# Performance work log

Measured on AMD Instinct MI355X. Metric: run time of the kernel, lower is better.

## Reference

```python
import jax, jax.numpy as jnp
import numpy as np

N_NODES = 100000
N_EDGES = 1600000
N_GRAPHS = 2000
F_IN = 16
HEADS = 8
C = 16            # per-head out channels (hidden_dim)
HC = HEADS * C    # 128
N_CLASSES = 2
NEG_SLOPE = 0.2   # PyG GATConv default leaky_relu slope


def setup_inputs() -> dict:
    key = jax.random.key(0)
    ks = jax.random.split(key, 12)
    x = jax.random.normal(ks[0], (N_NODES, F_IN), dtype=jnp.float32)
    edge_index = jax.random.randint(ks[1], (2, N_EDGES), 0, N_NODES, dtype=jnp.int32)
    batch = jnp.sort(jax.random.randint(ks[2], (N_NODES,), 0, N_GRAPHS, dtype=jnp.int32))
    s1 = 1.0 / np.sqrt(F_IN)
    s2 = 1.0 / np.sqrt(HC)
    return {
        "x": x,
        "edge_index": edge_index,
        "batch": batch,
        "W1": jax.random.normal(ks[3], (F_IN, HC), dtype=jnp.float32) * s1,
        "a1_src": jax.random.normal(ks[4], (HEADS, C), dtype=jnp.float32) * s2,
        "a1_dst": jax.random.normal(ks[5], (HEADS, C), dtype=jnp.float32) * s2,
        "b1": jnp.zeros((HC,), dtype=jnp.float32),
        "W2": jax.random.normal(ks[6], (HC, HC), dtype=jnp.float32) * s2,
        "a2_src": jax.random.normal(ks[7], (HEADS, C), dtype=jnp.float32) * s2,
        "a2_dst": jax.random.normal(ks[8], (HEADS, C), dtype=jnp.float32) * s2,
        "b2": jnp.zeros((HC,), dtype=jnp.float32),
        "lin_W": jax.random.normal(ks[9], (HC, N_CLASSES), dtype=jnp.float32) * s2,
        "lin_b": jnp.zeros((N_CLASSES,), dtype=jnp.float32),
    }


def gat_layer(h_in, src, dst, W, a_src, a_dst, b, num_nodes):
    # h: [N, H, C] per-head transformed features
    h = (h_in @ W).reshape(num_nodes, HEADS, C)
    # per-node attention half-logits: [N, H]
    logit_src = jnp.einsum('nhc,hc->nh', h, a_src)
    logit_dst = jnp.einsum('nhc,hc->nh', h, a_dst)
    # per-edge logits [E, H]
    e = jax.nn.leaky_relu(logit_src[src] + logit_dst[dst], NEG_SLOPE)
    # segment softmax over incoming edges of each destination node
    m = jax.ops.segment_max(e, dst, num_segments=num_nodes)
    m = jnp.where(jnp.isfinite(m), m, 0.0)
    ex = jnp.exp(e - m[dst])
    denom = jax.ops.segment_sum(ex, dst, num_segments=num_nodes)
    alpha = ex / jnp.maximum(denom[dst], 1e-16)
    # weighted scatter-add aggregation: [N, H, C]
    out = jax.ops.segment_sum(alpha[:, :, None] * h[src], dst, num_segments=num_nodes)
    return out.reshape(num_nodes, HC) + b


def reference(x, edge_index, batch, W1, a1_src, a1_dst, b1, W2, a2_src, a2_dst, b2, lin_W, lin_b):
    n = x.shape[0]
    # PyG GATConv adds self-loops by default
    loops = jnp.arange(n, dtype=edge_index.dtype)
    src = jnp.concatenate([edge_index[0], loops])
    dst = jnp.concatenate([edge_index[1], loops])
    h = jax.nn.relu(gat_layer(x, src, dst, W1, a1_src, a1_dst, b1, n))
    h = jax.nn.relu(gat_layer(h, src, dst, W2, a2_src, a2_dst, b2, n))
    # global mean pool per graph
    sums = jax.ops.segment_sum(h, batch, num_segments=N_GRAPHS)
    counts = jax.ops.segment_sum(jnp.ones((n, 1), h.dtype), batch, num_segments=N_GRAPHS)
    pooled = sums / jnp.maximum(counts, 1.0)
    logits = pooled @ lin_W + lin_b
    return jax.nn.softmax(logits, axis=1)
```

## Files before the change

kernel.cpp:

```cpp
#include <hip/hip_runtime.h>
#include <math.h>

#define N_NODES 100000
#define N_EDGESI 1600000
#define E_TOTAL (N_EDGESI + N_NODES)
#define N_GRAPHS 2000
#define F_IN 16
#define HEADS 8
#define CPH 16
#define HC 128
#define NEG 0.2f

#define BSHIFT 9
#define BNODES (1<<BSHIFT)
#define NBUK ((N_NODES + BNODES - 1)/BNODES)
#define BCAP 12288
#define BIN_EPT 8
#define BIN_TPB 256
#define BIN_EPB (BIN_EPT*BIN_TPB)
#define NBIN_BLK ((E_TOTAL + BIN_EPB - 1)/BIN_EPB)

#define GOFF_BLK ((N_NODES+255)/256)
#define WCONV_BLK ((HC*HC)/256)
#define XCONV_BLK ((N_NODES*4 + 255)/256)
#define W1CONV_BLK ((HC*32)/256)

typedef __bf16 bf16x8 __attribute__((ext_vector_type(8)));
typedef float  f32x4  __attribute__((ext_vector_type(4)));

__device__ __forceinline__ float leaky(float x){ return fmaxf(x, NEG*x); }
__device__ __forceinline__ float bf2f(unsigned short u){ return __uint_as_float(((unsigned)u)<<16); }
__device__ __forceinline__ unsigned short f2bf(float f){
  unsigned u = __float_as_uint(f);
  unsigned r = (u + 0x7fffu + ((u>>16)&1u)) >> 16;
  return (unsigned short)r;
}
__device__ __forceinline__ float blo(unsigned u){ return __uint_as_float(u<<16); }
__device__ __forceinline__ float bhi(unsigned u){ return __uint_as_float(u & 0xffff0000u); }

__global__ void k_pre(const int* __restrict__ ei, int* __restrict__ gpos, unsigned* __restrict__ gbin,
                      const int* __restrict__ batch, int* __restrict__ goff,
                      const float* __restrict__ W2, unsigned short* __restrict__ w2t,
                      const float* __restrict__ x, unsigned short* __restrict__ xbf,
                      const float* __restrict__ W1, unsigned short* __restrict__ w1t){
  int blk = blockIdx.x;
  if (blk < NBIN_BLK){
    __shared__ int cnt[NBUK];
    __shared__ int lofs[NBUK];
    __shared__ int bbase[NBUK];
    __shared__ int ws[4];
    __shared__ unsigned sorted[BIN_EPB];
    __shared__ unsigned short sbkt[BIN_EPB];
    int t = threadIdx.x;
    for (int i = t; i < NBUK; i += BIN_TPB) cnt[i] = 0;
    __syncthreads();
    int base = blk*BIN_EPB;
    unsigned entry[BIN_EPT]; int ebkt[BIN_EPT]; int erank[BIN_EPT];
    #pragma unroll
    for (int i = 0; i < BIN_EPT; ++i){
      int e = base + i*BIN_TPB + t;
      if (e < E_TOTAL){
        unsigned s, d;
        if (e < N_EDGESI){ s = (unsigned)ei[e]; d = (unsigned)ei[N_EDGESI + e]; }
        else { s = d = (unsigned)(e - N_EDGESI); }
        int b = (int)(d >> BSHIFT);
        erank[i] = atomicAdd(&cnt[b], 1);
        ebkt[i] = b;
        entry[i] = ((d & (BNODES-1u)) << 17) | s;
      } else ebkt[i] = -1;
    }
    __syncthreads();
    {
      int lane = t & 63, wv = t >> 6;
      int v = (t < NBUK) ? cnt[t] : 0;
      int sc = v;
      #pragma unroll
      for (int o = 1; o < 64; o <<= 1){ int u = __shfl_up(sc, o, 64); if (lane >= o) sc += u; }
      if (lane == 63) ws[wv] = sc;
      __syncthreads();
      if (wv == 0 && lane < 4){
        int w2v = ws[lane];
        #pragma unroll
        for (int o = 1; o < 4; o <<= 1){ int u = __shfl_up(w2v, o, 64); if (lane >= o) w2v += u; }
        ws[lane] = w2v;
      }
      __syncthreads();
      if (t < NBUK){
        lofs[t] = (wv ? ws[wv-1] : 0) + sc - v;
        bbase[t] = v ? atomicAdd(&gpos[t], v) : 0;
      }
    }
    __syncthreads();
    #pragma unroll
    for (int i = 0; i < BIN_EPT; ++i){
      if (ebkt[i] >= 0){
        int p = lofs[ebkt[i]] + erank[i];
        sorted[p] = entry[i];
        sbkt[p] = (unsigned short)ebkt[i];
      }
    }
    __syncthreads();
    int nval = E_TOTAL - base; if (nval > BIN_EPB) nval = BIN_EPB;
    for (int i = t; i < nval; i += BIN_TPB){
      int b = sbkt[i];
      gbin[(size_t)b*BCAP + bbase[b] + (i - lofs[b])] = sorted[i];
    }
  } else if (blk < NBIN_BLK + GOFF_BLK){
    int n = (blk - NBIN_BLK)*256 + threadIdx.x;
    if (n >= N_NODES) return;
    int b = batch[n];
    if (n == 0){ for (int g = 0; g <= b; ++g) goff[g] = 0; }
    int b1 = (n+1 < N_NODES) ? batch[n+1] : N_GRAPHS;
    for (int g = b+1; g <= b1; ++g) goff[g] = n+1;
  } else if (blk < NBIN_BLK + GOFF_BLK + WCONV_BLK){
    int i = (blk - NBIN_BLK - GOFF_BLK)*256 + threadIdx.x;
    if (i >= HC*HC) return;
    int c = i >> 7, k = i & 127;
    w2t[i] = f2bf(W2[k*HC + c]);
  } else if (blk < NBIN_BLK + GOFF_BLK + WCONV_BLK + XCONV_BLK){
    int p = (blk - NBIN_BLK - GOFF_BLK - WCONV_BLK)*256 + threadIdx.x;
    if (p >= N_NODES*4) return;
    int n = p >> 2, q = p & 3;
    float4 xv = ((const float4*)(x + n*F_IN))[q];
    ushort4 o; o.x = f2bf(xv.x); o.y = f2bf(xv.y); o.z = f2bf(xv.z); o.w = f2bf(xv.w);
    ((ushort4*)(xbf + (size_t)n*32))[q] = o;
    ushort4 z; z.x = 0; z.y = 0; z.z = 0; z.w = 0;
    ((ushort4*)(xbf + (size_t)n*32 + 16))[q] = z;
  } else {
    int i = (blk - NBIN_BLK - GOFF_BLK - WCONV_BLK - XCONV_BLK)*256 + threadIdx.x;
    if (i >= HC*32) return;
    int c = i >> 5, k = i & 31;
    w1t[i] = (k < F_IN) ? f2bf(W1[k*HC + c]) : (unsigned short)0;
  }
}

__global__ __launch_bounds__(512) void k_csr(
                      const int* __restrict__ gpos, const unsigned* __restrict__ gbin,
                      int* __restrict__ off, int* __restrict__ csrc){
  __shared__ int lcnt[BNODES];
  __shared__ int wsum[8];
  __shared__ int gp[NBUK];
  __shared__ int sbase;
  int b = blockIdx.x, t = threadIdx.x;
  for (int i = t; i < NBUK; i += 512) gp[i] = gpos[i];
  lcnt[t] = 0;
  __syncthreads();
  if (t == 0){ int s = 0; for (int j = 0; j < b; ++j) s += gp[j]; sbase = s; }
  int nb = gp[b];
  const unsigned* bb = gbin + (size_t)b*BCAP;
  __syncthreads();
  int base = sbase;
  for (int i = t; i < nb; i += 512) atomicAdd(&lcnt[bb[i] >> 17], 1);
  __syncthreads();
  int lane = t & 63, wv = t >> 6;
  int v = lcnt[t];
  int sc = v;
  #pragma unroll
  for (int o = 1; o < 64; o <<= 1){ int u = __shfl_up(sc, o, 64); if (lane >= o) sc += u; }
  if (lane == 63) wsum[wv] = sc;
  __syncthreads();
  if (wv == 0 && lane < 8){
    int w2 = wsum[lane];
    #pragma unroll
    for (int o = 1; o < 8; o <<= 1){ int u = __shfl_up(w2, o, 64); if (lane >= o) w2 += u; }
    wsum[lane] = w2;
  }
  __syncthreads();
  int excl = (wv ? wsum[wv-1] : 0) + sc - v;
  int d = (b << BSHIFT) + t;
  if (d < N_NODES) off[d] = base + excl;
  if (b == NBUK-1 && t == 0) off[N_NODES] = E_TOTAL;
  __syncthreads();
  lcnt[t] = base + excl;
  __syncthreads();
  for (int i = t; i < nb; i += 512){
    unsigned en = bb[i];
    int p = atomicAdd(&lcnt[en >> 17], 1);
    csrc[p] = (int)(en & 0x1ffffu);
  }
}

template<int KS>
__global__ __launch_bounds__(256) void k_gemm_mfma(
                             const unsigned short* __restrict__ hin,
                             const unsigned short* __restrict__ wt,
                             const float* __restrict__ asrc, const float* __restrict__ adst,
                             unsigned short* __restrict__ hb,
                             float* __restrict__ ls, float* __restrict__ ld){
  __shared__ unsigned short hls[64][132];
  const int KST = KS*32;
  int t = threadIdx.x, lane = t & 63, wv = t >> 6;
  int n0 = blockIdx.x*64 + wv*16;
  int rowl = lane & 15, kgrp = lane >> 4;
  int row = n0 + rowl;
  int rowc = (row < N_NODES) ? row : (N_NODES-1);
  bf16x8 a[KS];
  #pragma unroll
  for (int ks = 0; ks < KS; ++ks)
    a[ks] = *(const bf16x8*)(hin + (size_t)rowc*KST + ks*32 + kgrp*8);
  #pragma unroll
  for (int ct = 0; ct < 8; ++ct){
    f32x4 acc = {0.f, 0.f, 0.f, 0.f};
    int col = ct*16 + rowl;
    #pragma unroll
    for (int ks = 0; ks < KS; ++ks){
      bf16x8 b = *(const bf16x8*)(wt + (size_t)col*KST + ks*32 + kgrp*8);
      acc = __builtin_amdgcn_mfma_f32_16x16x32_bf16(a[ks], b, acc, 0, 0, 0);
    }
    #pragma unroll
    for (int r = 0; r < 4; ++r){
      int lrow = wv*16 + kgrp*4 + r;
      int ro = n0 + kgrp*4 + r;
      unsigned short hv = f2bf(acc[r]);
      hls[lrow][col] = hv;
      if (ro < N_NODES) hb[(size_t)ro*HC + col] = hv;
    }
  }
  __syncthreads();
  #pragma unroll
  for (int pp = 0; pp < 2; ++pp){
    int p = t + pp*256;
    int lrow = p >> 3, h = p & 7;
    int gn = blockIdx.x*64 + lrow;
    if (gn < N_NODES){
      const unsigned short* rp = &hls[lrow][h*16];
      uint2 A = *(const uint2*)rp;
      uint2 B = *(const uint2*)(rp+4);
      uint2 C = *(const uint2*)(rp+8);
      uint2 D = *(const uint2*)(rp+12);
      float c[16] = { blo(A.x), bhi(A.x), blo(A.y), bhi(A.y),
                      blo(B.x), bhi(B.x), blo(B.y), bhi(B.y),
                      blo(C.x), bhi(C.x), blo(C.y), bhi(C.y),
                      blo(D.x), bhi(D.x), blo(D.y), bhi(D.y) };
      const float* as = asrc + h*CPH;
      const float* ad = adst + h*CPH;
      float s0 = 0.f, s1 = 0.f;
      #pragma unroll
      for (int q = 0; q < 16; ++q){ s0 += c[q]*as[q]; s1 += c[q]*ad[q]; }
      ls[gn*8 + h] = s0;
      ld[gn*8 + h] = s1;
    }
  }
}

__global__ void k_agg(const int* __restrict__ off, const int* __restrict__ csrc,
                      const unsigned short* __restrict__ hb, const float* __restrict__ ls,
                      const float* __restrict__ ld, const float* __restrict__ bias,
                      unsigned short* __restrict__ outb){
  int wid = threadIdx.x >> 6, lane = threadIdx.x & 63;
  int n = blockIdx.x*4 + wid;
  if (n >= N_NODES) return;
  int rs = __builtin_amdgcn_readfirstlane(off[n]);
  int re = __builtin_amdgcn_readfirstlane(off[n+1]);
  int q = lane >> 4;
  int l = lane & 15;
  int h = l >> 1;
  float ldh = ld[n*8 + h];
  const uint4* hb4 = (const uint4*)hb;
  float ac0=0.f, ac1=0.f, ac2=0.f, ac3=0.f, ac4=0.f, ac5=0.f, ac6=0.f, ac7=0.f, dsum=0.f;
  #define AGG_BODY(J) { \
    int s = __shfl(sv, (J), 64); \
    float g = ls[s*8 + h]; \
    float ex = __expf(leaky(g + ldh)); \
    uint4 v = hb4[(size_t)s*16 + l]; \
    ac0 += ex*blo(v.x); ac1 += ex*bhi(v.x); \
    ac2 += ex*blo(v.y); ac3 += ex*bhi(v.y); \
    ac4 += ex*blo(v.z); ac5 += ex*bhi(v.z); \
    ac6 += ex*blo(v.w); ac7 += ex*bhi(v.w); \
    dsum += ex; }
  int nb = re - rs;
  for (int cb = 0; cb < nb; cb += 64){
    int cnt = nb - cb; if (cnt > 64) cnt = 64;
    int sv = csrc[rs + cb + (lane < cnt ? lane : 0)];
    int jj = 0;
    for (; jj + 16 <= cnt; jj += 16){
      AGG_BODY(jj+q) AGG_BODY(jj+q+4) AGG_BODY(jj+q+8) AGG_BODY(jj+q+12)
    }
    for (int j = jj + q; j < cnt; j += 4) AGG_BODY(j)
  }
  #undef AGG_BODY
  ac0 += __shfl_xor(ac0,16,64); ac0 += __shfl_xor(ac0,32,64);
  ac1 += __shfl_xor(ac1,16,64); ac1 += __shfl_xor(ac1,32,64);
  ac2 += __shfl_xor(ac2,16,64); ac2 += __shfl_xor(ac2,32,64);
  ac3 += __shfl_xor(ac3,16,64); ac3 += __shfl_xor(ac3,32,64);
  ac4 += __shfl_xor(ac4,16,64); ac4 += __shfl_xor(ac4,32,64);
  ac5 += __shfl_xor(ac5,16,64); ac5 += __shfl_xor(ac5,32,64);
  ac6 += __shfl_xor(ac6,16,64); ac6 += __shfl_xor(ac6,32,64);
  ac7 += __shfl_xor(ac7,16,64); ac7 += __shfl_xor(ac7,32,64);
  dsum += __shfl_xor(dsum,16,64); dsum += __shfl_xor(dsum,32,64);
  if (q == 0){
    float inv = 1.f/fmaxf(dsum, 1e-16f);
    float4 b0 = ((const float4*)bias)[l*2];
    float4 b1 = ((const float4*)bias)[l*2+1];
    uint4 o;
    o.x = (unsigned)f2bf(fmaxf(ac0*inv + b0.x, 0.f)) | ((unsigned)f2bf(fmaxf(ac1*inv + b0.y, 0.f)) << 16);
    o.y = (unsigned)f2bf(fmaxf(ac2*inv + b0.z, 0.f)) | ((unsigned)f2bf(fmaxf(ac3*inv + b0.w, 0.f)) << 16);
    o.z = (unsigned)f2bf(fmaxf(ac4*inv + b1.x, 0.f)) | ((unsigned)f2bf(fmaxf(ac5*inv + b1.y, 0.f)) << 16);
    o.w = (unsigned)f2bf(fmaxf(ac6*inv + b1.z, 0.f)) | ((unsigned)f2bf(fmaxf(ac7*inv + b1.w, 0.f)) << 16);
    ((uint4*)outb)[(size_t)n*16 + l] = o;
  }
}

__global__ void k_poolcls(const unsigned short* __restrict__ h, const int* __restrict__ goff,
                          const float* __restrict__ lw, const float* __restrict__ lb,
                          float* __restrict__ out){
  __shared__ float sh[4][HC];
  int g = blockIdx.x;
  int t = threadIdx.x, lane = t & 63, wv = t >> 6;
  int s = goff[g], epos = goff[g+1];
  float a0 = 0.f, a1 = 0.f;
  const ushort2* h2 = (const ushort2*)h;
  for (int n = s + wv; n < epos; n += 4){
    ushort2 v = h2[(size_t)n*64 + lane];
    a0 += bf2f(v.x); a1 += bf2f(v.y);
  }
  sh[wv][lane*2] = a0; sh[wv][lane*2+1] = a1;
  __syncthreads();
  if (wv == 0){
    int c0 = lane*2;
    float p0 = sh[0][c0] + sh[1][c0] + sh[2][c0] + sh[3][c0];
    float p1 = sh[0][c0+1] + sh[1][c0+1] + sh[2][c0+1] + sh[3][c0+1];
    int cntg = epos - s;
    float invc = 1.f/fmaxf((float)cntg, 1.f);
    float v0 = p0*invc, v1 = p1*invc;
    float l0 = v0*lw[c0*2+0] + v1*lw[(c0+1)*2+0];
    float l1 = v0*lw[c0*2+1] + v1*lw[(c0+1)*2+1];
    #pragma unroll
    for (int o = 32; o >= 1; o >>= 1){ l0 += __shfl_xor(l0,o,64); l1 += __shfl_xor(l1,o,64); }
    if (lane == 0){
      l0 += lb[0]; l1 += lb[1];
      float m = fmaxf(l0,l1);
      float e0 = __expf(l0-m), e1 = __expf(l1-m);
      float si = e0 + e1;
      out[g*2]   = e0/si;
      out[g*2+1] = e1/si;
    }
  }
}

extern "C" void kernel_launch(void* const* d_in, const int* in_sizes, int n_in,
                              void* d_out, int out_size, void* d_ws, size_t ws_size,
                              hipStream_t stream){
  const float* x   = (const float*)d_in[0];
  const int*   ei  = (const int*)d_in[1];
  const int*   bat = (const int*)d_in[2];
  const float* W1  = (const float*)d_in[3];
  const float* a1s = (const float*)d_in[4];
  const float* a1d = (const float*)d_in[5];
  const float* b1  = (const float*)d_in[6];
  const float* W2  = (const float*)d_in[7];
  const float* a2s = (const float*)d_in[8];
  const float* a2d = (const float*)d_in[9];
  const float* b2  = (const float*)d_in[10];
  const float* lw  = (const float*)d_in[11];
  const float* lb  = (const float*)d_in[12];
  float* out = (float*)d_out;

  char* w = (char*)d_ws;
  auto alloc = [&](size_t bytes)->void*{ void* p = (void*)w; w += (bytes + 511) & ~size_t(511); return p; };
  int* off    = (int*)alloc((size_t)(N_NODES+1)*4);
  int* csrc   = (int*)alloc((size_t)E_TOTAL*4);
  int* goff   = (int*)alloc((size_t)(N_GRAPHS+1)*4);
  int* gpos   = (int*)alloc((size_t)NBUK*4);
  unsigned* gbin = (unsigned*)alloc((size_t)NBUK*BCAP*4);
  unsigned short* w2t  = (unsigned short*)alloc((size_t)HC*HC*2);
  unsigned short* w1t  = (unsigned short*)alloc((size_t)HC*32*2);
  unsigned short* xbf  = (unsigned short*)alloc((size_t)N_NODES*32*2);
  unsigned short* hbf  = (unsigned short*)alloc((size_t)N_NODES*HC*2);
  unsigned short* hbf2 = (unsigned short*)alloc((size_t)N_NODES*HC*2);
  float* lsb  = (float*)alloc((size_t)N_NODES*HEADS*4);
  float* ldb  = (float*)alloc((size_t)N_NODES*HEADS*4);

  hipMemsetAsync(gpos, 0, (size_t)NBUK*4, stream);

  k_pre  <<<NBIN_BLK + GOFF_BLK + WCONV_BLK + XCONV_BLK + W1CONV_BLK,BIN_TPB,0,stream>>>(
           ei, gpos, gbin, bat, goff, W2, w2t, x, xbf, W1, w1t);
  k_gemm_mfma<1><<<(N_NODES+63)/64,256,0,stream>>>(xbf, w1t, a1s, a1d, hbf, lsb, ldb);
  k_csr  <<<NBUK,512,0,stream>>>(gpos, gbin, off, csrc);

  k_agg  <<<(N_NODES+3)/4,256,0,stream>>>(off, csrc, hbf, lsb, ldb, b1, hbf2);
  k_gemm_mfma<4><<<(N_NODES+63)/64,256,0,stream>>>(hbf2, w2t, a2s, a2d, hbf, lsb, ldb);
  k_agg  <<<(N_NODES+3)/4,256,0,stream>>>(off, csrc, hbf, lsb, ldb, b2, hbf2);

  k_poolcls<<<N_GRAPHS,256,0,stream>>>(hbf2, goff, lw, lb, out);
}
```

Before: 270.1 us.

## Replace LDS-sorted edge binning with two-pass count-then-scatter, more edges per block

Edge binning is restructured. Each block now counts bucket sizes in one pass, reserves global space per bucket, then re-reads the edge indices and writes each edge straight to its global bin slot using a shared-memory rank atomic. This drops the shared-memory staging sort and the prefix scan, and raises edges per thread from 8 to 32 so there are fewer blocks and fewer global gpos atomics. In exchange, edge_index is read twice and the global writes within a block are no longer grouped by bucket, which may make them less coalesced.

```diff
diff --git a/kernel.cpp b/kernel.cpp
--- a/kernel.cpp
+++ b/kernel.cpp
@@ -15,7 +15,7 @@
 #define BNODES (1<<BSHIFT)
 #define NBUK ((N_NODES + BNODES - 1)/BNODES)
 #define BCAP 12288
-#define BIN_EPT 8
+#define BIN_EPT 32
 #define BIN_TPB 256
 #define BIN_EPB (BIN_EPT*BIN_TPB)
 #define NBIN_BLK ((E_TOTAL + BIN_EPB - 1)/BIN_EPB)
@@ -46,17 +46,27 @@
   int blk = blockIdx.x;
   if (blk < NBIN_BLK){
     __shared__ int cnt[NBUK];
-    __shared__ int lofs[NBUK];
+    __shared__ int rnk[NBUK];
     __shared__ int bbase[NBUK];
-    __shared__ int ws[4];
-    __shared__ unsigned sorted[BIN_EPB];
-    __shared__ unsigned short sbkt[BIN_EPB];
     int t = threadIdx.x;
-    for (int i = t; i < NBUK; i += BIN_TPB) cnt[i] = 0;
+    for (int i = t; i < NBUK; i += BIN_TPB){ cnt[i] = 0; rnk[i] = 0; }
     __syncthreads();
     int base = blk*BIN_EPB;
-    unsigned entry[BIN_EPT]; int ebkt[BIN_EPT]; int erank[BIN_EPT];
-    #pragma unroll
+    #pragma unroll 4
+    for (int i = 0; i < BIN_EPT; ++i){
+      int e = base + i*BIN_TPB + t;
+      if (e < E_TOTAL){
+        unsigned d = (e < N_EDGESI) ? (unsigned)ei[N_EDGESI + e] : (unsigned)(e - N_EDGESI);
+        atomicAdd(&cnt[d >> BSHIFT], 1);
+      }
+    }
+    __syncthreads();
+    for (int i = t; i < NBUK; i += BIN_TPB){
+      int v = cnt[i];
+      bbase[i] = v ? atomicAdd(&gpos[i], v) : 0;
+    }
+    __syncthreads();
+    #pragma unroll 4
     for (int i = 0; i < BIN_EPT; ++i){
       int e = base + i*BIN_TPB + t;
       if (e < E_TOTAL){
@@ -64,46 +74,9 @@
         if (e < N_EDGESI){ s = (unsigned)ei[e]; d = (unsigned)ei[N_EDGESI + e]; }
         else { s = d = (unsigned)(e - N_EDGESI); }
         int b = (int)(d >> BSHIFT);
-        erank[i] = atomicAdd(&cnt[b], 1);
-        ebkt[i] = b;
-        entry[i] = ((d & (BNODES-1u)) << 17) | s;
-      } else ebkt[i] = -1;
-    }
-    __syncthreads();
-    {
-      int lane = t & 63, wv = t >> 6;
-      int v = (t < NBUK) ? cnt[t] : 0;
-      int sc = v;
-      #pragma unroll
-      for (int o = 1; o < 64; o <<= 1){ int u = __shfl_up(sc, o, 64); if (lane >= o) sc += u; }
-      if (lane == 63) ws[wv] = sc;
-      __syncthreads();
-      if (wv == 0 && lane < 4){
-        int w2v = ws[lane];
-        #pragma unroll
-        for (int o = 1; o < 4; o <<= 1){ int u = __shfl_up(w2v, o, 64); if (lane >= o) w2v += u; }
-        ws[lane] = w2v;
+        int r = atomicAdd(&rnk[b], 1);
+        gbin[(size_t)b*BCAP + bbase[b] + r] = ((d & (BNODES-1u)) << 17) | s;
       }
-      __syncthreads();
-      if (t < NBUK){
-        lofs[t] = (wv ? ws[wv-1] : 0) + sc - v;
-        bbase[t] = v ? atomicAdd(&gpos[t], v) : 0;
-      }
-    }
-    __syncthreads();
-    #pragma unroll
-    for (int i = 0; i < BIN_EPT; ++i){
-      if (ebkt[i] >= 0){
-        int p = lofs[ebkt[i]] + erank[i];
-        sorted[p] = entry[i];
-        sbkt[p] = (unsigned short)ebkt[i];
-      }
-    }
-    __syncthreads();
-    int nval = E_TOTAL - base; if (nval > BIN_EPB) nval = BIN_EPB;
-    for (int i = t; i < nval; i += BIN_TPB){
-      int b = sbkt[i];
-      gbin[(size_t)b*BCAP + bbase[b] + (i - lofs[b])] = sorted[i];
     }
   } else if (blk < NBIN_BLK + GOFF_BLK){
     int n = (blk - NBIN_BLK)*256 + threadIdx.x;
```

New measurement: 274.9 us. Within noise of the previous version (+1.8%).

## Split CSR build into per-quarter count, global scan and scatter kernels

Applied to the files above, without the earlier changes.

Replaces the single per-bucket CSR kernel (196 blocks of 512 threads) with four-way split count and scatter kernels plus a three-pass global prefix scan over per-split counts. The aim is more parallelism than about 196 blocks give on a large GPU, and removing the serial per-block prefix over bucket sizes. It adds four extra kernel launches and extra global traffic for the count and prefix arrays (about 400K ints each).

```diff
diff --git a/kernel.cpp b/kernel.cpp
--- a/kernel.cpp
+++ b/kernel.cpp
@@ -10,6 +10,7 @@
 #define CPH 16
 #define HC 128
 #define NEG 0.2f
+#define SCAN_B 1024
 
 #define BSHIFT 9
 #define BNODES (1<<BSHIFT)
@@ -19,6 +20,9 @@
 #define BIN_TPB 256
 #define BIN_EPB (BIN_EPT*BIN_TPB)
 #define NBIN_BLK ((E_TOTAL + BIN_EPB - 1)/BIN_EPB)
+#define CSR_SPLIT 4
+#define CNT4_LEN (NBUK*BNODES*CSR_SPLIT)
+#define NB_SCAN4 ((CNT4_LEN + SCAN_B - 1)/SCAN_B)
 
 #define GOFF_BLK ((N_NODES+255)/256)
 #define WCONV_BLK ((HC*HC)/256)
@@ -134,49 +138,94 @@
   }
 }
 
-__global__ __launch_bounds__(512) void k_csr(
-                      const int* __restrict__ gpos, const unsigned* __restrict__ gbin,
-                      int* __restrict__ off, int* __restrict__ csrc){
-  __shared__ int lcnt[BNODES];
-  __shared__ int wsum[8];
-  __shared__ int gp[NBUK];
-  __shared__ int sbase;
-  int b = blockIdx.x, t = threadIdx.x;
-  for (int i = t; i < NBUK; i += 512) gp[i] = gpos[i];
-  lcnt[t] = 0;
-  __syncthreads();
-  if (t == 0){ int s = 0; for (int j = 0; j < b; ++j) s += gp[j]; sbase = s; }
-  int nb = gp[b];
+__global__ void k_cnt4(const int* __restrict__ gpos, const unsigned* __restrict__ gbin,
+                       int* __restrict__ cnt4){
+  __shared__ int lc[BNODES];
+  int b = blockIdx.x >> 2, p = blockIdx.x & 3;
+  int t = threadIdx.x;
+  for (int i = t; i < BNODES; i += 256) lc[i] = 0;
+  __syncthreads();
+  int nb = gpos[b];
+  int lo = (int)(((long long)nb*p)/CSR_SPLIT);
+  int hi = (int)(((long long)nb*(p+1))/CSR_SPLIT);
   const unsigned* bb = gbin + (size_t)b*BCAP;
-  __syncthreads();
-  int base = sbase;
-  for (int i = t; i < nb; i += 512) atomicAdd(&lcnt[bb[i] >> 17], 1);
-  __syncthreads();
-  int lane = t & 63, wv = t >> 6;
-  int v = lcnt[t];
+  for (int i = lo + t; i < hi; i += 256) atomicAdd(&lc[bb[i] >> 17], 1);
+  __syncthreads();
+  int base = (b << BSHIFT)*CSR_SPLIT + p;
+  for (int i = t; i < BNODES; i += 256) cnt4[base + i*CSR_SPLIT] = lc[i];
+}
+
+__global__ void k_scan1(const int* __restrict__ cnt, int* __restrict__ ps, int* __restrict__ bsum){
+  __shared__ int ws[16];
+  int b = blockIdx.x, t = threadIdx.x, lane = t & 63, wv = t >> 6;
+  int i = b*SCAN_B + t;
+  int v = (i < CNT4_LEN) ? cnt[i] : 0;
   int sc = v;
   #pragma unroll
-  for (int o = 1; o < 64; o <<= 1){ int u = __shfl_up(sc, o, 64); if (lane >= o) sc += u; }
-  if (lane == 63) wsum[wv] = sc;
-  __syncthreads();
-  if (wv == 0 && lane < 8){
-    int w2 = wsum[lane];
-    #pragma unroll
-    for (int o = 1; o < 8; o <<= 1){ int u = __shfl_up(w2, o, 64); if (lane >= o) w2 += u; }
-    wsum[lane] = w2;
-  }
-  __syncthreads();
-  int excl = (wv ? wsum[wv-1] : 0) + sc - v;
-  int d = (b << BSHIFT) + t;
-  if (d < N_NODES) off[d] = base + excl;
-  if (b == NBUK-1 && t == 0) off[N_NODES] = E_TOTAL;
-  __syncthreads();
-  lcnt[t] = base + excl;
-  __syncthreads();
-  for (int i = t; i < nb; i += 512){
+  for (int o=1;o<64;o<<=1){ int u = __shfl_up(sc, o, 64); if (lane >= o) sc += u; }
+  if (lane==63) ws[wv] = sc;
+  __syncthreads();
+  if (wv==0 && lane<16){
+    int w = ws[lane];
+    #pragma unroll
+    for (int o=1;o<16;o<<=1){ int u = __shfl_up(w,o,64); if (lane>=o) w += u; }
+    ws[lane] = w;
+  }
+  __syncthreads();
+  int base = wv ? ws[wv-1] : 0;
+  if (i < CNT4_LEN) ps[i] = base + sc - v;
+  if (t == SCAN_B-1) bsum[b] = ws[15];
+}
+
+__global__ void k_scan2(int* __restrict__ bsum, int nb){
+  __shared__ int ws[8];
+  int t = threadIdx.x, lane = t & 63, wv = t >> 6;
+  int v = (t < nb) ? bsum[t] : 0;
+  int sc = v;
+  #pragma unroll
+  for (int o=1;o<64;o<<=1){ int u = __shfl_up(sc,o,64); if (lane>=o) sc += u; }
+  if (lane==63) ws[wv] = sc;
+  __syncthreads();
+  if (wv==0 && lane<8){
+    int w = ws[lane];
+    #pragma unroll
+    for (int o=1;o<8;o<<=1){ int u = __shfl_up(w,o,64); if (lane>=o) w += u; }
+    ws[lane] = w;
+  }
+  __syncthreads();
+  int base = wv ? ws[wv-1] : 0;
+  if (t < nb) bsum[t] = base + sc - v;
+}
+
+__global__ void k_scan3(int* __restrict__ ps, const int* __restrict__ bsum, int* __restrict__ offc){
+  int i = blockIdx.x*256 + threadIdx.x;
+  if (i < CNT4_LEN){
+    int v = ps[i] + bsum[i>>10];
+    ps[i] = v;
+    if ((i & 3) == 0){
+      int n = i >> 2;
+      if (n < N_NODES) offc[n] = v;
+    }
+  }
+  if (i == 0) offc[N_NODES] = E_TOTAL;
+}
+
+__global__ void k_scat4(const int* __restrict__ gpos, const unsigned* __restrict__ gbin,
+                        const int* __restrict__ ps, int* __restrict__ csrc){
+  __shared__ int lcur[BNODES];
+  int b = blockIdx.x >> 2, p = blockIdx.x & 3;
+  int t = threadIdx.x;
+  int base = (b << BSHIFT)*CSR_SPLIT + p;
+  for (int i = t; i < BNODES; i += 256) lcur[i] = ps[base + i*CSR_SPLIT];
+  __syncthreads();
+  int nb = gpos[b];
+  int lo = (int)(((long long)nb*p)/CSR_SPLIT);
+  int hi = (int)(((long long)nb*(p+1))/CSR_SPLIT);
+  const unsigned* bb = gbin + (size_t)b*BCAP;
+  for (int i = lo + t; i < hi; i += 256){
     unsigned en = bb[i];
-    int p = atomicAdd(&lcnt[en >> 17], 1);
-    csrc[p] = (int)(en & 0x1ffffu);
+    int pos = atomicAdd(&lcur[en >> 17], 1);
+    csrc[pos] = (int)(en & 0x1ffffu);
   }
 }
 
@@ -358,7 +407,10 @@
 
   char* w = (char*)d_ws;
   auto alloc = [&](size_t bytes)->void*{ void* p = (void*)w; w += (bytes + 511) & ~size_t(511); return p; };
-  int* off    = (int*)alloc((size_t)(N_NODES+1)*4);
+  int* offc   = (int*)alloc((size_t)(N_NODES+1)*4);
+  int* cnt4   = (int*)alloc((size_t)CNT4_LEN*4);
+  int* psum   = (int*)alloc((size_t)CNT4_LEN*4);
+  int* bsum   = (int*)alloc((size_t)(NB_SCAN4+1)*4);
   int* csrc   = (int*)alloc((size_t)E_TOTAL*4);
   int* goff   = (int*)alloc((size_t)(N_GRAPHS+1)*4);
   int* gpos   = (int*)alloc((size_t)NBUK*4);
@@ -375,12 +427,16 @@
 
   k_pre  <<<NBIN_BLK + GOFF_BLK + WCONV_BLK + XCONV_BLK + W1CONV_BLK,BIN_TPB,0,stream>>>(
            ei, gpos, gbin, bat, goff, W2, w2t, x, xbf, W1, w1t);
+  k_cnt4 <<<NBUK*CSR_SPLIT,256,0,stream>>>(gpos, gbin, cnt4);
+  k_scan1<<<NB_SCAN4,SCAN_B,0,stream>>>(cnt4, psum, bsum);
+  k_scan2<<<1,512,0,stream>>>(bsum, NB_SCAN4);
+  k_scan3<<<(CNT4_LEN+255)/256,256,0,stream>>>(psum, bsum, offc);
   k_gemm_mfma<1><<<(N_NODES+63)/64,256,0,stream>>>(xbf, w1t, a1s, a1d, hbf, lsb, ldb);
-  k_csr  <<<NBUK,512,0,stream>>>(gpos, gbin, off, csrc);
-
-  k_agg  <<<(N_NODES+3)/4,256,0,stream>>>(off, csrc, hbf, lsb, ldb, b1, hbf2);
+  k_scat4<<<NBUK*CSR_SPLIT,256,0,stream>>>(gpos, gbin, psum, csrc);
+
+  k_agg  <<<(N_NODES+3)/4,256,0,stream>>>(offc, csrc, hbf, lsb, ldb, b1, hbf2);
   k_gemm_mfma<4><<<(N_NODES+63)/64,256,0,stream>>>(hbf2, w2t, a2s, a2d, hbf, lsb, ldb);
-  k_agg  <<<(N_NODES+3)/4,256,0,stream>>>(off, csrc, hbf, lsb, ldb, b2, hbf2);
+  k_agg  <<<(N_NODES+3)/4,256,0,stream>>>(offc, csrc, hbf, lsb, ldb, b2, hbf2);
 
   k_poolcls<<<N_GRAPHS,256,0,stream>>>(hbf2, goff, lw, lb, out);
 }
```

Result: slower. 287.5 us (+6.4%).
